# Optimization experiments

Hardware: AMD Instinct MI355X
Metric: run time of the kernel (lower is better)

The kernel has to match this reference:

```python
import jax, jax.numpy as jnp
import numpy as np

B, S, D = 2, 2048, 1024
H, DK, DV = 16, 64, 64
EPS = 1e-5
SQRT_DK = float(np.sqrt(DK))


def setup_inputs() -> dict:
    key = jax.random.key(0)
    ks = jax.random.split(key, 8)
    sc = 0.02
    return {
        "x": jax.random.normal(ks[0], (B, S, D), jnp.float32),
        "Wk": jax.random.normal(ks[1], (D, H * DK), jnp.float32) * sc,
        "bk": jnp.zeros((H * DK,), jnp.float32),
        "Wq": jax.random.normal(ks[2], (D, H * DK), jnp.float32) * sc,
        "bq": jnp.zeros((H * DK,), jnp.float32),
        "Wv": jax.random.normal(ks[3], (D, H * DV), jnp.float32) * sc,
        "bv": jnp.zeros((H * DV,), jnp.float32),
        "Wo": jax.random.normal(ks[4], (H * DV, D), jnp.float32) * sc,
        "bo": jnp.zeros((D,), jnp.float32),
        "gamma": jnp.ones((D,), jnp.float32),
        "beta": jnp.zeros((D,), jnp.float32),
    }


def reference(x, Wk, bk, Wq, bq, Wv, bv, Wo, bo, gamma, beta):
    b, s, d = x.shape
    # NOTE: original torch code reshapes (B, S, H*dk) directly to (B, H, S, dk)
    # without a transpose; we replicate that exact (non-standard) reshape.
    keys = (x @ Wk + bk).reshape(b, H, s, DK)
    queries = (x @ Wq + bq).reshape(b, H, s, DK)
    values = (x @ Wv + bv).reshape(b, H, s, DV)

    scores = jnp.einsum('bhqd,bhkd->bhqk', queries, keys) / SQRT_DK
    causal_mask = jnp.triu(jnp.ones((s, s), bool), k=1)  # True = masked
    scores = jnp.where(causal_mask[None, None], jnp.float32(-1e9), scores)
    attention = jax.nn.softmax(scores, axis=-1)

    context = jnp.einsum('bhqk,bhkd->bhqd', attention, values)
    context = context.reshape(b, s, H * DV)

    out = context @ Wo + bo  # dropout is identity at inference
    out = out + x            # residual connection

    mean = jnp.mean(out, axis=-1, keepdims=True)
    var = jnp.mean(jnp.square(out - mean), axis=-1, keepdims=True)
    return (out - mean) / jnp.sqrt(var + EPS) * gamma + beta
```

## Files before the change

### kernel.cpp

```cpp
#include <hip/hip_runtime.h>


typedef __attribute__((ext_vector_type(8))) __bf16 bf16x8;
typedef __attribute__((ext_vector_type(8))) unsigned short ushort8;
typedef __attribute__((ext_vector_type(4))) unsigned short u16x4;
typedef __attribute__((ext_vector_type(4))) float f32x4;

static __device__ __forceinline__ unsigned short f2bf(float f) {
    unsigned u = __builtin_bit_cast(unsigned, f);
    u += 0x7fffu + ((u >> 16) & 1u);
    return (unsigned short)(u >> 16);
}

__global__ __launch_bounds__(256) void cast_kernel(const float* __restrict__ src,
                                                   unsigned short* __restrict__ dst, int n4) {
    int i = blockIdx.x * 256 + threadIdx.x;
    if (i >= n4) return;
    float4 v = ((const float4*)src)[i];
    ushort4 o;
    o.x = f2bf(v.x); o.y = f2bf(v.y); o.z = f2bf(v.z); o.w = f2bf(v.w);
    ((ushort4*)dst)[i] = o;
}

__global__ __launch_bounds__(256) void castT_kernel(const float* __restrict__ src,
                                                    unsigned short* __restrict__ dst) {
    __shared__ __align__(16) unsigned short t[64 * 68];
    const int tid = threadIdx.x;
    const int n0 = blockIdx.x * 64, k0 = blockIdx.y * 64;
    #pragma unroll
    for (int u = 0; u < 4; u++) {
        int e = u * 256 + tid;
        int r = e >> 4, c4 = (e & 15) * 4;
        float4 v = *(const float4*)(src + (k0 + r) * 1024 + n0 + c4);
        ushort4 o;
        o.x = f2bf(v.x); o.y = f2bf(v.y); o.z = f2bf(v.z); o.w = f2bf(v.w);
        *(ushort4*)(t + r * 68 + c4) = o;
    }
    __syncthreads();
    #pragma unroll
    for (int u = 0; u < 4; u++) {
        int e = u * 256 + tid;
        int rn = e >> 4, ck = (e & 15) * 4;
        ushort4 o;
        o.x = t[(ck + 0) * 68 + rn];
        o.y = t[(ck + 1) * 68 + rn];
        o.z = t[(ck + 2) * 68 + rn];
        o.w = t[(ck + 3) * 68 + rn];
        *(ushort4*)(dst + (n0 + rn) * 1024 + k0 + ck) = o;
    }
}

__global__ __launch_bounds__(256) void vtrans_kernel(const unsigned short* __restrict__ V,
                                                     unsigned short* __restrict__ VT) {
    __shared__ __align__(16) unsigned short t[64 * 68];
    const int tid = threadIdx.x;
    const int p0 = blockIdx.x * 64;
    const long base = (long)blockIdx.y * 131072;
    #pragma unroll
    for (int u = 0; u < 2; u++) {
        int e = u * 256 + tid;
        int r = e >> 3, c8 = (e & 7) * 8;
        ushort8 v = *(const ushort8*)(V + base + (long)(p0 + r) * 64 + c8);
        *(ushort8*)(t + r * 68 + c8) = v;
    }
    __syncthreads();
    #pragma unroll
    for (int u = 0; u < 4; u++) {
        int e = u * 256 + tid;
        int dv = e >> 4, pk = (e & 15) * 4;
        ushort4 o;
        o.x = t[(pk + 0) * 68 + dv];
        o.y = t[(pk + 1) * 68 + dv];
        o.z = t[(pk + 2) * 68 + dv];
        o.w = t[(pk + 3) * 68 + dv];
        *(ushort4*)(VT + base + (long)dv * 2048 + p0 + pk) = o;
    }
}

__global__ __launch_bounds__(256, 3) void gemm_kernel(
    const unsigned short* __restrict__ A,
    const unsigned short* __restrict__ Bt,
    const float* __restrict__ b0, const float* __restrict__ b1, const float* __restrict__ b2,
    unsigned short* __restrict__ outQ, unsigned short* __restrict__ outK,
    unsigned short* __restrict__ outV,
    float* __restrict__ outF, const float* __restrict__ resid, int mode)
{
    __shared__ __align__(16) unsigned short As[2][128 * 32];
    __shared__ __align__(16) unsigned short Bs[2][128 * 32];
    const int tid = threadIdx.x;
    const int lane = tid & 63, wave = tid >> 6;
    const int quad = lane >> 4, l16 = lane & 15;
    const int wm = wave >> 1, wn = wave & 1;
    const int row0 = blockIdx.y * 128, n0g = blockIdx.x * 128;

    const int sr = tid >> 2;
    const int sc = (tid & 3) * 8;
    const unsigned short* Ag0 = A + (size_t)(row0 + sr) * 1024 + sc;
    const unsigned short* Ag1 = A + (size_t)(row0 + 64 + sr) * 1024 + sc;
    const unsigned short* Bg0 = Bt + (size_t)(n0g + sr) * 1024 + sc;
    const unsigned short* Bg1 = Bt + (size_t)(n0g + 64 + sr) * 1024 + sc;

    {
        ushort8 a0 = *(const ushort8*)(Ag0);
        ushort8 a1 = *(const ushort8*)(Ag1);
        ushort8 bv0 = *(const ushort8*)(Bg0);
        ushort8 bv1 = *(const ushort8*)(Bg1);
        *(ushort8*)(As[0] + sr * 32 + sc) = a0;
        *(ushort8*)(As[0] + (64 + sr) * 32 + sc) = a1;
        *(ushort8*)(Bs[0] + sr * 32 + sc) = bv0;
        *(ushort8*)(Bs[0] + (64 + sr) * 32 + sc) = bv1;
    }
    __syncthreads();

    f32x4 acc[4][4] = {};
    #pragma unroll 2
    for (int it = 0; it < 32; ++it) {
        const int cur = it & 1;
        ushort8 na0, na1, nb0, nb1;
        if (it < 31) {
            const int k0 = (it + 1) * 32;
            na0 = *(const ushort8*)(Ag0 + k0);
            na1 = *(const ushort8*)(Ag1 + k0);
            nb0 = *(const ushort8*)(Bg0 + k0);
            nb1 = *(const ushort8*)(Bg1 + k0);
        }
        bf16x8 af[4], bfr[4];
        #pragma unroll
        for (int i = 0; i < 4; i++)
            af[i] = *(const bf16x8*)(As[cur] + (wm * 64 + i * 16 + l16) * 32 + quad * 8);
        #pragma unroll
        for (int j = 0; j < 4; j++)
            bfr[j] = *(const bf16x8*)(Bs[cur] + (wn * 64 + j * 16 + l16) * 32 + quad * 8);
        #pragma unroll
        for (int i = 0; i < 4; i++)
            #pragma unroll
            for (int j = 0; j < 4; j++)
                acc[i][j] = __builtin_amdgcn_mfma_f32_16x16x32_bf16(af[i], bfr[j], acc[i][j], 0, 0, 0);
        if (it < 31) {
            const int nxt = cur ^ 1;
            *(ushort8*)(As[nxt] + sr * 32 + sc) = na0;
            *(ushort8*)(As[nxt] + (64 + sr) * 32 + sc) = na1;
            *(ushort8*)(Bs[nxt] + sr * 32 + sc) = nb0;
            *(ushort8*)(Bs[nxt] + (64 + sr) * 32 + sc) = nb1;
            __syncthreads();
        }
    }

    if (mode == 0) {
        const int which = n0g >> 10;
        const float* bp = (which == 0) ? b0 : (which == 1) ? b1 : b2;
        unsigned short* op = (which == 0) ? outQ : (which == 1) ? outK : outV;
        const float scl = (which == 0) ? 0.125f : 1.0f;
        #pragma unroll
        for (int i = 0; i < 4; i++)
            #pragma unroll
            for (int j = 0; j < 4; j++) {
                int c = (n0g + wn * 64 + j * 16 + l16) & 1023;
                float bj = bp[c];
                #pragma unroll
                for (int r = 0; r < 4; r++) {
                    int r_g = row0 + wm * 64 + i * 16 + quad * 4 + r;
                    op[(size_t)r_g * 1024 + c] = f2bf((acc[i][j][r] + bj) * scl);
                }
            }
    } else {
        #pragma unroll
        for (int i = 0; i < 4; i++)
            #pragma unroll
            for (int j = 0; j < 4; j++) {
                int c_g = n0g + wn * 64 + j * 16 + l16;
                float bj = b0[c_g];
                #pragma unroll
                for (int r = 0; r < 4; r++) {
                    int r_g = row0 + wm * 64 + i * 16 + quad * 4 + r;
                    size_t idx = (size_t)r_g * 1024 + c_g;
                    outF[idx] = acc[i][j][r] + bj + resid[idx];
                }
            }
    }
}

__global__ __launch_bounds__(256, 3) void flash_kernel(
    const unsigned short* __restrict__ Q,
    const unsigned short* __restrict__ K,
    const unsigned short* __restrict__ VT,
    unsigned short* __restrict__ Ctx)
{
    __shared__ __align__(16) unsigned short Kt[128 * 72];
    __shared__ __align__(16) unsigned short Vt[64 * 136];
    __shared__ __align__(16) unsigned short Pt[4][16 * 136];
    const int tid = threadIdx.x;
    const int lane = tid & 63, wave = tid >> 6;
    const int quad = lane >> 4, l16 = lane & 15;
    const int qb = 31 - blockIdx.y;
    const int q0 = qb * 64;
    const long base = (long)blockIdx.x * 131072;

    bf16x8 qa[2];
    #pragma unroll
    for (int kk = 0; kk < 2; kk++)
        qa[kk] = *(const bf16x8*)(Q + base + (q0 + wave * 16 + l16) * 64 + kk * 32 + quad * 8);

    f32x4 o[4] = {};
    float l_one = 0.f;
    const int nt = (qb + 2) >> 1;
    const int qpos = q0 + wave * 16 + l16;

    #pragma unroll
    for (int u = 0; u < 4; u++) {
        int e = u * 256 + tid;
        int r = e >> 3, c = (e & 7) * 8;
        *(ushort8*)(Kt + r * 72 + c) = *(const ushort8*)(K + base + (long)r * 64 + c);
        int dv = e >> 4, kc = (e & 15) * 8;
        *(ushort8*)(Vt + dv * 136 + kc) = *(const ushort8*)(VT + base + (long)dv * 2048 + kc);
    }
    __syncthreads();

    for (int t = 0; t < nt; t++) {
        ushort8 nk[4], nv[4];
        if (t + 1 < nt) {
            const int k1 = (t + 1) * 128;
            #pragma unroll
            for (int u = 0; u < 4; u++) {
                int e = u * 256 + tid;
                int r = e >> 3, c = (e & 7) * 8;
                nk[u] = *(const ushort8*)(K + base + (long)(k1 + r) * 64 + c);
                int dv = e >> 4, kc = (e & 15) * 8;
                nv[u] = *(const ushort8*)(VT + base + (long)dv * 2048 + k1 + kc);
            }
        }
        const int k0 = t * 128;
        const int climit = (q0 + 63 - k0) >> 4;
        const bool diag = (t == nt - 1);
        unsigned short* pw = Pt[wave];

        #pragma unroll
        for (int c = 0; c < 8; c++) {
            u16x4 pk4 = {};
            if (c <= climit) {
                bf16x8 kb0 = *(const bf16x8*)(Kt + (c * 16 + l16) * 72 + quad * 8);
                bf16x8 kb1 = *(const bf16x8*)(Kt + (c * 16 + l16) * 72 + 32 + quad * 8);
                f32x4 a = {};
                a = __builtin_amdgcn_mfma_f32_16x16x32_bf16(kb0, qa[0], a, 0, 0, 0);
                a = __builtin_amdgcn_mfma_f32_16x16x32_bf16(kb1, qa[1], a, 0, 0, 0);
                #pragma unroll
                for (int r = 0; r < 4; r++) {
                    float p = __expf(a[r]);
                    if (diag) {
                        int kpos = k0 + c * 16 + quad * 4 + r;
                        p = (kpos > qpos) ? 0.f : p;
                    }
                    a[r] = p;
                }
                l_one += (a[0] + a[1]) + (a[2] + a[3]);
                pk4[0] = f2bf(a[0]); pk4[1] = f2bf(a[1]);
                pk4[2] = f2bf(a[2]); pk4[3] = f2bf(a[3]);
            }
            *(u16x4*)(pw + l16 * 136 + c * 16 + quad * 4) = pk4;
        }

        const int kkmax = (climit >> 1) < 3 ? (climit >> 1) : 3;
        #pragma unroll
        for (int kk = 0; kk < 4; kk++) {
            if (kk <= kkmax) {
                bf16x8 pa = *(const bf16x8*)(pw + l16 * 136 + kk * 32 + quad * 8);
                #pragma unroll
                for (int c2 = 0; c2 < 4; c2++) {
                    bf16x8 vb = *(const bf16x8*)(Vt + (c2 * 16 + l16) * 136 + kk * 32 + quad * 8);
                    o[c2] = __builtin_amdgcn_mfma_f32_16x16x32_bf16(pa, vb, o[c2], 0, 0, 0);
                }
            }
        }
        __syncthreads();
        if (t + 1 < nt) {
            #pragma unroll
            for (int u = 0; u < 4; u++) {
                int e = u * 256 + tid;
                int r = e >> 3, c = (e & 7) * 8;
                *(ushort8*)(Kt + r * 72 + c) = nk[u];
                int dv = e >> 4, kc = (e & 15) * 8;
                *(ushort8*)(Vt + dv * 136 + kc) = nv[u];
            }
            __syncthreads();
        }
    }

    l_one += __shfl_xor(l_one, 16, 64);
    l_one += __shfl_xor(l_one, 32, 64);
    float rinv[4];
    #pragma unroll
    for (int r = 0; r < 4; r++)
        rinv[r] = 1.0f / __shfl(l_one, quad * 4 + r, 16);
    #pragma unroll
    for (int c2 = 0; c2 < 4; c2++)
        #pragma unroll
        for (int r = 0; r < 4; r++) {
            int row = q0 + wave * 16 + quad * 4 + r;
            Ctx[base + (long)row * 64 + c2 * 16 + l16] = f2bf(o[c2][r] * rinv[r]);
        }
}

__global__ __launch_bounds__(256) void ln_kernel(const float* __restrict__ inp,
                                                 const float* __restrict__ gamma,
                                                 const float* __restrict__ beta,
                                                 float* __restrict__ out)
{
    __shared__ float ssum[4], ssq[4];
    const int row = blockIdx.x;
    const int tid = threadIdx.x;
    float4 v = ((const float4*)(inp + (size_t)row * 1024))[tid];
    float s = v.x + v.y + v.z + v.w;
    float q = v.x * v.x + v.y * v.y + v.z * v.z + v.w * v.w;
    #pragma unroll
    for (int off = 32; off >= 1; off >>= 1) {
        s += __shfl_xor(s, off, 64);
        q += __shfl_xor(q, off, 64);
    }
    if ((tid & 63) == 0) { ssum[tid >> 6] = s; ssq[tid >> 6] = q; }
    __syncthreads();
    float ts = ssum[0] + ssum[1] + ssum[2] + ssum[3];
    float tq = ssq[0] + ssq[1] + ssq[2] + ssq[3];
    float mean = ts * (1.f / 1024.f);
    float var = tq * (1.f / 1024.f) - mean * mean;
    float rinv = rsqrtf(var + 1e-5f);
    float4 g = ((const float4*)gamma)[tid];
    float4 b = ((const float4*)beta)[tid];
    float4 o;
    o.x = (v.x - mean) * rinv * g.x + b.x;
    o.y = (v.y - mean) * rinv * g.y + b.y;
    o.z = (v.z - mean) * rinv * g.z + b.z;
    o.w = (v.w - mean) * rinv * g.w + b.w;
    ((float4*)(out + (size_t)row * 1024))[tid] = o;
}

extern "C" void kernel_launch(void* const* d_in, const int* in_sizes, int n_in,
                              void* d_out, int out_size, void* d_ws, size_t ws_size,
                              hipStream_t stream) {
    const float* x     = (const float*)d_in[0];
    const float* Wk    = (const float*)d_in[1];
    const float* bk    = (const float*)d_in[2];
    const float* Wq    = (const float*)d_in[3];
    const float* bq    = (const float*)d_in[4];
    const float* Wv    = (const float*)d_in[5];
    const float* bv    = (const float*)d_in[6];
    const float* Wo    = (const float*)d_in[7];
    const float* bo    = (const float*)d_in[8];
    const float* gamma = (const float*)d_in[9];
    const float* beta  = (const float*)d_in[10];
    float* out = (float*)d_out;

    char* ws = (char*)d_ws;
    unsigned short* xb    = (unsigned short*)(ws);
    unsigned short* WqkvT = (unsigned short*)(ws + (8ull << 20));
    unsigned short* WoT   = (unsigned short*)(ws + (14ull << 20));
    unsigned short* Qb    = (unsigned short*)(ws + (16ull << 20));
    unsigned short* Kb    = (unsigned short*)(ws + (24ull << 20));
    unsigned short* VbT   = (unsigned short*)(ws + (32ull << 20));
    unsigned short* Cb    = (unsigned short*)(ws + (40ull << 20));
    float* outp           = (float*)(ws + (48ull << 20));
    unsigned short* Vbn   = Cb;

    cast_kernel<<<4096, 256, 0, stream>>>(x, xb, 1048576);
    dim3 tgrid(16, 16);
    castT_kernel<<<tgrid, 256, 0, stream>>>(Wq, WqkvT);
    castT_kernel<<<tgrid, 256, 0, stream>>>(Wk, WqkvT + (1u << 20));
    castT_kernel<<<tgrid, 256, 0, stream>>>(Wv, WqkvT + (2u << 20));
    castT_kernel<<<tgrid, 256, 0, stream>>>(Wo, WoT);

    dim3 qkvgrid(24, 32);
    gemm_kernel<<<qkvgrid, 256, 0, stream>>>(xb, WqkvT, bq, bk, bv,
                                             Qb, Kb, Vbn, nullptr, nullptr, 0);

    dim3 vgrid(32, 32);
    vtrans_kernel<<<vgrid, 256, 0, stream>>>(Vbn, VbT);

    dim3 fgrid(32, 32);
    flash_kernel<<<fgrid, 256, 0, stream>>>(Qb, Kb, VbT, Cb);

    dim3 ogrid(8, 32);
    gemm_kernel<<<ogrid, 256, 0, stream>>>(Cb, WoT, bo, nullptr, nullptr,
                                           nullptr, nullptr, nullptr, outp, x, 1);

    ln_kernel<<<4096, 256, 0, stream>>>(outp, gamma, beta, out);
}
```

Baseline: 208.1 us.

## Merge cast/transpose prep into one launch and store pre-LN output as bf16

Replaces five separate prep launches (x cast plus four weight cast-transposes) with a single 3D-grid prep kernel, cutting launch overhead and letting the work run concurrently. Separately, the output projection now writes its residual-added result as bf16 instead of fp32, and the layernorm reads bf16, halving that intermediate's traffic. In exchange, the layernorm input loses precision because the fp32 residual sum is rounded to bf16 before mean and variance are computed.

```diff
diff --git a/kernel.cpp b/kernel.cpp
--- a/kernel.cpp
+++ b/kernel.cpp
@@ -12,20 +12,34 @@
     return (unsigned short)(u >> 16);
 }
 
-__global__ __launch_bounds__(256) void cast_kernel(const float* __restrict__ src,
-                                                   unsigned short* __restrict__ dst, int n4) {
-    int i = blockIdx.x * 256 + threadIdx.x;
-    if (i >= n4) return;
-    float4 v = ((const float4*)src)[i];
-    ushort4 o;
-    o.x = f2bf(v.x); o.y = f2bf(v.y); o.z = f2bf(v.z); o.w = f2bf(v.w);
-    ((ushort4*)dst)[i] = o;
-}
-
-__global__ __launch_bounds__(256) void castT_kernel(const float* __restrict__ src,
-                                                    unsigned short* __restrict__ dst) {
+static __device__ __forceinline__ float bf2f(unsigned short u) {
+    return __builtin_bit_cast(float, (unsigned)u << 16);
+}
+
+__global__ __launch_bounds__(256) void prep_kernel(
+    const float* __restrict__ x,
+    const float* __restrict__ Wq, const float* __restrict__ Wk,
+    const float* __restrict__ Wv, const float* __restrict__ Wo,
+    unsigned short* __restrict__ xb, unsigned short* __restrict__ WT)
+{
+    const int tid = threadIdx.x;
+    const int z = blockIdx.z;
+    if (z == 4) {
+        const int bid = blockIdx.y * 16 + blockIdx.x;
+        const int base = bid * 4096 + tid;
+        #pragma unroll
+        for (int it = 0; it < 16; it++) {
+            int i = base + it * 256;
+            float4 v = ((const float4*)x)[i];
+            ushort4 o;
+            o.x = f2bf(v.x); o.y = f2bf(v.y); o.z = f2bf(v.z); o.w = f2bf(v.w);
+            ((ushort4*)xb)[i] = o;
+        }
+        return;
+    }
+    const float* src = (z == 0) ? Wq : (z == 1) ? Wk : (z == 2) ? Wv : Wo;
+    unsigned short* dst = WT + ((size_t)z << 20);
     __shared__ __align__(16) unsigned short t[64 * 68];
-    const int tid = threadIdx.x;
     const int n0 = blockIdx.x * 64, k0 = blockIdx.y * 64;
     #pragma unroll
     for (int u = 0; u < 4; u++) {
@@ -83,7 +97,7 @@
     const float* __restrict__ b0, const float* __restrict__ b1, const float* __restrict__ b2,
     unsigned short* __restrict__ outQ, unsigned short* __restrict__ outK,
     unsigned short* __restrict__ outV,
-    float* __restrict__ outF, const float* __restrict__ resid, int mode)
+    const float* __restrict__ resid, int mode)
 {
     __shared__ __align__(16) unsigned short As[2][128 * 32];
     __shared__ __align__(16) unsigned short Bs[2][128 * 32];
@@ -174,7 +188,7 @@
                 for (int r = 0; r < 4; r++) {
                     int r_g = row0 + wm * 64 + i * 16 + quad * 4 + r;
                     size_t idx = (size_t)r_g * 1024 + c_g;
-                    outF[idx] = acc[i][j][r] + bj + resid[idx];
+                    outQ[idx] = f2bf(acc[i][j][r] + bj + resid[idx]);
                 }
             }
     }
@@ -300,7 +314,7 @@
         }
 }
 
-__global__ __launch_bounds__(256) void ln_kernel(const float* __restrict__ inp,
+__global__ __launch_bounds__(256) void ln_kernel(const unsigned short* __restrict__ inp,
                                                  const float* __restrict__ gamma,
                                                  const float* __restrict__ beta,
                                                  float* __restrict__ out)
@@ -308,9 +322,10 @@
     __shared__ float ssum[4], ssq[4];
     const int row = blockIdx.x;
     const int tid = threadIdx.x;
-    float4 v = ((const float4*)(inp + (size_t)row * 1024))[tid];
-    float s = v.x + v.y + v.z + v.w;
-    float q = v.x * v.x + v.y * v.y + v.z * v.z + v.w * v.w;
+    ushort4 uv = ((const ushort4*)(inp + (size_t)row * 1024))[tid];
+    float vx = bf2f(uv.x), vy = bf2f(uv.y), vz = bf2f(uv.z), vw = bf2f(uv.w);
+    float s = vx + vy + vz + vw;
+    float q = vx * vx + vy * vy + vz * vz + vw * vw;
     #pragma unroll
     for (int off = 32; off >= 1; off >>= 1) {
         s += __shfl_xor(s, off, 64);
@@ -326,10 +341,10 @@
     float4 g = ((const float4*)gamma)[tid];
     float4 b = ((const float4*)beta)[tid];
     float4 o;
-    o.x = (v.x - mean) * rinv * g.x + b.x;
-    o.y = (v.y - mean) * rinv * g.y + b.y;
-    o.z = (v.z - mean) * rinv * g.z + b.z;
-    o.w = (v.w - mean) * rinv * g.w + b.w;
+    o.x = (vx - mean) * rinv * g.x + b.x;
+    o.y = (vy - mean) * rinv * g.y + b.y;
+    o.z = (vz - mean) * rinv * g.z + b.z;
+    o.w = (vw - mean) * rinv * g.w + b.w;
     ((float4*)(out + (size_t)row * 1024))[tid] = o;
 }
 
@@ -352,24 +367,20 @@
     char* ws = (char*)d_ws;
     unsigned short* xb    = (unsigned short*)(ws);
     unsigned short* WqkvT = (unsigned short*)(ws + (8ull << 20));
-    unsigned short* WoT   = (unsigned short*)(ws + (14ull << 20));
     unsigned short* Qb    = (unsigned short*)(ws + (16ull << 20));
     unsigned short* Kb    = (unsigned short*)(ws + (24ull << 20));
     unsigned short* VbT   = (unsigned short*)(ws + (32ull << 20));
     unsigned short* Cb    = (unsigned short*)(ws + (40ull << 20));
-    float* outp           = (float*)(ws + (48ull << 20));
+    unsigned short* outp  = (unsigned short*)(ws + (48ull << 20));
+    unsigned short* WoT   = WqkvT + (3u << 20);
     unsigned short* Vbn   = Cb;
 
-    cast_kernel<<<4096, 256, 0, stream>>>(x, xb, 1048576);
-    dim3 tgrid(16, 16);
-    castT_kernel<<<tgrid, 256, 0, stream>>>(Wq, WqkvT);
-    castT_kernel<<<tgrid, 256, 0, stream>>>(Wk, WqkvT + (1u << 20));
-    castT_kernel<<<tgrid, 256, 0, stream>>>(Wv, WqkvT + (2u << 20));
-    castT_kernel<<<tgrid, 256, 0, stream>>>(Wo, WoT);
+    dim3 pgrid(16, 16, 5);
+    prep_kernel<<<pgrid, 256, 0, stream>>>(x, Wq, Wk, Wv, Wo, xb, WqkvT);
 
     dim3 qkvgrid(24, 32);
     gemm_kernel<<<qkvgrid, 256, 0, stream>>>(xb, WqkvT, bq, bk, bv,
-                                             Qb, Kb, Vbn, nullptr, nullptr, 0);
+                                             Qb, Kb, Vbn, nullptr, 0);
 
     dim3 vgrid(32, 32);
     vtrans_kernel<<<vgrid, 256, 0, stream>>>(Vbn, VbT);
@@ -379,7 +390,7 @@
 
     dim3 ogrid(8, 32);
     gemm_kernel<<<ogrid, 256, 0, stream>>>(Cb, WoT, bo, nullptr, nullptr,
-                                           nullptr, nullptr, nullptr, outp, x, 1);
+                                           outp, nullptr, nullptr, x, 1);
 
     ln_kernel<<<4096, 256, 0, stream>>>(outp, gamma, beta, out);
 }
```

After: 200.2 us. -3.8%, faster.
